# Performance work log

Measured on AMD Instinct MI355X. Metric: run time of the kernel, lower is better.

Reference implementation:

```python
import jax, jax.numpy as jnp
import numpy as np

N_NODES = 100000
N_EDGES = 1600000
N_FEAT = 128
N_HID = 128
N_CLS = 40
DROP_P = 0.5


def setup_inputs() -> dict:
    key = jax.random.key(0)
    k1, k2, k3, k4 = jax.random.split(key, 4)
    x = jax.random.normal(k1, (N_NODES, N_FEAT), dtype=jnp.float32)
    edge_index = jax.random.randint(k2, (2, N_EDGES), 0, N_NODES, dtype=jnp.int32)
    W1 = jax.random.normal(k3, (N_FEAT, N_HID), dtype=jnp.float32) / np.sqrt(N_FEAT)
    b1 = jnp.zeros((N_HID,), dtype=jnp.float32)
    W2 = jax.random.normal(k4, (N_HID, N_CLS), dtype=jnp.float32) / np.sqrt(N_HID)
    b2 = jnp.zeros((N_CLS,), dtype=jnp.float32)
    return {"x": x, "edge_index": edge_index, "W1": W1, "b1": b1, "W2": W2, "b2": b2}


def _gcn_norm(edge_index, num_nodes):
    # add self-loops, then symmetric normalization D^-1/2 (A+I) D^-1/2
    loops = jnp.arange(num_nodes, dtype=edge_index.dtype)
    src = jnp.concatenate([edge_index[0], loops])
    dst = jnp.concatenate([edge_index[1], loops])
    deg = jax.ops.segment_sum(jnp.ones_like(dst, dtype=jnp.float32), dst,
                              num_segments=num_nodes)
    deg_isqrt = jax.lax.rsqrt(deg)  # deg >= 1 thanks to self-loops
    norm = deg_isqrt[src] * deg_isqrt[dst]  # [E+N]
    return src, dst, norm


def _gcn_conv(x, src, dst, norm, W, b, num_nodes):
    h = x @ W                                   # [N, out]
    msg = h[src] * norm[:, None]                # gather + scale, [E+N, out]
    out = jax.ops.segment_sum(msg, dst, num_segments=num_nodes)  # scatter-add
    return out + b


def reference(x, edge_index, W1, b1, W2, b2):
    num_nodes = x.shape[0]
    src, dst, norm = _gcn_norm(edge_index, num_nodes)
    h = _gcn_conv(x, src, dst, norm, W1, b1, num_nodes)
    h = jax.nn.relu(h)
    # dropout(p=0.5, training=True) with a fixed key for determinism
    keep = jax.random.uniform(jax.random.key(42), h.shape) >= DROP_P
    h = jnp.where(keep, h / (1.0 - DROP_P), 0.0)
    out = _gcn_conv(h, src, dst, norm, W2, b2, num_nodes)
    return out
```

## Files before the change

### kernel.cpp

```cpp
#include <hip/hip_runtime.h>

#define N_NODES 100000
#define N_EDGES 1600000
#define NBUCK 196
#define G1B 1563
#define FB 391
#define FEDGE 4096
#define BCAP 9216

typedef __attribute__((ext_vector_type(8))) short short8v;
typedef __attribute__((ext_vector_type(4))) float f32x4;

__device__ __forceinline__ unsigned pack_bf16(float a, float b){
  unsigned ua = __float_as_uint(a), ub = __float_as_uint(b);
  ua = ua + 0x7fffu + ((ua >> 16) & 1u);
  ub = ub + 0x7fffu + ((ub >> 16) & 1u);
  return (ua >> 16) | (ub & 0xffff0000u);
}
__device__ __forceinline__ unsigned short bf16_of(float a){
  unsigned ua = __float_as_uint(a);
  ua = ua + 0x7fffu + ((ua >> 16) & 1u);
  return (unsigned short)(ua >> 16);
}
__device__ __forceinline__ float bf_lo(unsigned u){ return __uint_as_float(u << 16); }
__device__ __forceinline__ float bf_hi(unsigned u){ return __uint_as_float(u & 0xffff0000u); }

__device__ __forceinline__ unsigned tf_rotl(unsigned x, int r){ return (x<<r)|(x>>(32-r)); }

__device__ __forceinline__ unsigned dropout_keep(unsigned e){
  unsigned x0 = 0u, x1 = e;
  const unsigned k0 = 0u, k1v = 42u;
  const unsigned k2 = 0x1BD11BDAu ^ k0 ^ k1v;
#define TF_R(r) { x0 += x1; x1 = tf_rotl(x1,(r)); x1 ^= x0; }
  x0 += k0; x1 += k1v;
  TF_R(13) TF_R(15) TF_R(26) TF_R(6)
  x0 += k1v; x1 += k2 + 1u;
  TF_R(17) TF_R(29) TF_R(16) TF_R(24)
  x0 += k2; x1 += k0 + 2u;
  TF_R(13) TF_R(15) TF_R(26) TF_R(6)
  x0 += k0; x1 += k1v + 3u;
  TF_R(17) TF_R(29) TF_R(16) TF_R(24)
  x0 += k1v; x1 += k2 + 4u;
  TF_R(13) TF_R(15) TF_R(26) TF_R(6)
  x0 += k2; x1 += k0 + 5u;
#undef TF_R
  return (x0 ^ x1) >> 31;
}

__global__ void k_init(const float* __restrict__ W1, const float* __restrict__ W2,
                       unsigned short* __restrict__ W1T, unsigned short* __restrict__ W2T48,
                       int* __restrict__ bcur2){
  int b = blockIdx.x, t = threadIdx.x;
  if (b < 64){
    int idx = b*256 + t;
    int k = idx >> 7, n = idx & 127;
    W1T[n*128 + k] = bf16_of(W1[idx]);
  } else {
    if (t < NBUCK) bcur2[t] = 0;
    for (int i = t; i < 48*128; i += 256){
      int c = i >> 7, k = i & 127;
      W2T48[c*128 + k] = (c < 40) ? bf16_of(W2[k*40 + c]) : (unsigned short)0;
    }
  }
}

__launch_bounds__(256)
__global__ void k_B(const float* __restrict__ x, const unsigned short* __restrict__ W1T,
                    unsigned short* __restrict__ h1u,
                    const int* __restrict__ src, const int* __restrict__ dst,
                    int* __restrict__ bcur2, unsigned* __restrict__ tmp, int N, int E){
  __shared__ int hist[NBUCK];
  int t = threadIdx.x;
  if (blockIdx.x < FB){
    int fb = blockIdx.x;
    for (int i = t; i < NBUCK; i += 256) hist[i] = 0;
    __syncthreads();
    int e0 = fb*FEDGE;
    #pragma unroll 4
    for (int j = 0; j < FEDGE/256; j++){
      int e = e0 + t + j*256;
      if (e < E) atomicAdd(&hist[dst[e] >> 9], 1);
    }
    __syncthreads();
    if (t < NBUCK){
      int c = hist[t];
      if (c > 0) hist[t] = t*BCAP + atomicAdd(&bcur2[t], c);
    }
    __syncthreads();
    #pragma unroll 4
    for (int j = 0; j < FEDGE/256; j++){
      int e = e0 + t + j*256;
      if (e < E){
        int d = dst[e], s = src[e];
        int p = atomicAdd(&hist[d >> 9], 1);
        tmp[p] = ((unsigned)(d & 511) << 17) | (unsigned)s;
      }
    }
    return;
  }
  int gb = blockIdx.x - FB;
  if (gb >= G1B) return;
  int w = t >> 6, l = t & 63;
  int lo = l & 15, hi = l >> 4;
  int rowA = gb*64 + w*16 + lo;
  int rA = (rowA < N) ? rowA : (N-1);
  const float4* xr = (const float4*)(x + (size_t)rA*128);

  short8v a[4];
  #pragma unroll
  for (int kk = 0; kk < 4; kk++){
    float4 f0 = xr[kk*8 + 2*hi];
    float4 f1 = xr[kk*8 + 2*hi + 1];
    union { short8v v; unsigned u[4]; } A;
    A.u[0] = pack_bf16(f0.x, f0.y);
    A.u[1] = pack_bf16(f0.z, f0.w);
    A.u[2] = pack_bf16(f1.x, f1.y);
    A.u[3] = pack_bf16(f1.z, f1.w);
    a[kk] = A.v;
  }
  int rowC0 = gb*64 + w*16 + hi*4;
  #pragma unroll
  for (int tt = 0; tt < 8; tt++){
    int n0 = tt*16;
    const uint4* brow = (const uint4*)(W1T + (n0 + lo)*128);
    f32x4 acc = {0.f, 0.f, 0.f, 0.f};
    #pragma unroll
    for (int kk = 0; kk < 4; kk++){
      union { short8v v; uint4 q; } B;
      B.q = brow[kk*4 + hi];
      acc = __builtin_amdgcn_mfma_f32_16x16x32_bf16(a[kk], B.v, acc, 0, 0, 0);
    }
    int colC = n0 + lo;
    #pragma unroll
    for (int r = 0; r < 4; r++){
      int rc = rowC0 + r;
      if (rc < N) h1u[(size_t)rc*128 + colC] = bf16_of(acc[r]);
    }
  }
}

__launch_bounds__(1024)
__global__ void k_sort(const unsigned* __restrict__ tmp, const int* __restrict__ bcur2,
                       int* __restrict__ degi, int* __restrict__ off,
                       float* __restrict__ dii, unsigned* __restrict__ csr, int N){
  __shared__ int cur[512];
  __shared__ int wtot[8];
  int b = blockIdx.x, t = threadIdx.x;
  if (t < 512) cur[t] = 0;
  __syncthreads();
  int m = bcur2[b];
  int base = b*BCAP;
  int node0 = b << 9;
  for (int i = t; i < m; i += 1024)
    atomicAdd(&cur[tmp[base + i] >> 17], 1);
  __syncthreads();
  int v = 0, excl = 0;
  if (t < 512){
    v = cur[t];
    int lane = t & 63, w = t >> 6;
    int incl = v;
    for (int d = 1; d < 64; d <<= 1){
      int y = __shfl_up(incl, d);
      if (lane >= d) incl += y;
    }
    if (lane == 63) wtot[w] = incl;
    __syncthreads();
    int wb = 0;
    for (int i = 0; i < w; i++) wb += wtot[i];
    excl = wb + incl - v;
    int n = node0 + t;
    if (n < N){
      degi[n] = v;
      off[n]  = base + excl;
      dii[n]  = rsqrtf((float)(v + 1));
    }
  } else {
    __syncthreads();
  }
  __syncthreads();
  if (t < 512) cur[t] = base + excl;
  __syncthreads();
  for (int i = t; i < m; i += 1024){
    unsigned e = tmp[base + i];
    int dloc = e >> 17;
    int p = atomicAdd(&cur[dloc], 1);
    csr[p] = e & 0x1FFFFu;
  }
}

__launch_bounds__(256)
__global__ void k_agg1(const unsigned* __restrict__ h1g, unsigned* __restrict__ Bbg,
                       const unsigned* __restrict__ csr, const int* __restrict__ off,
                       const int* __restrict__ degi, const float* __restrict__ dii,
                       const float* __restrict__ b1, int N){
  int n = blockIdx.x*4 + (threadIdx.x >> 6);
  int lane = threadIdx.x & 63;
  if (n >= N) return;
  n = __builtin_amdgcn_readfirstlane(n);
  float din = dii[n];
  float s2 = din*din;
  unsigned su = h1g[(size_t)n*64 + lane];
  float a0 = bf_lo(su)*s2, a1 = bf_hi(su)*s2;
  int o = off[n], cnt = degi[n];
  int i = 0;
  for (; i + 8 <= cnt; i += 8){
    unsigned s0 = csr[o+i+0], s1 = csr[o+i+1], s2i = csr[o+i+2], s3 = csr[o+i+3];
    unsigned s4 = csr[o+i+4], s5 = csr[o+i+5], s6 = csr[o+i+6], s7 = csr[o+i+7];
    float w0 = dii[s0]*din, w1 = dii[s1]*din, w2 = dii[s2i]*din, w3 = dii[s3]*din;
    float w4 = dii[s4]*din, w5 = dii[s5]*din, w6 = dii[s6]*din, w7 = dii[s7]*din;
    unsigned u0 = h1g[(size_t)s0*64 + lane];
    unsigned u1 = h1g[(size_t)s1*64 + lane];
    unsigned u2 = h1g[(size_t)s2i*64 + lane];
    unsigned u3 = h1g[(size_t)s3*64 + lane];
    unsigned u4 = h1g[(size_t)s4*64 + lane];
    unsigned u5 = h1g[(size_t)s5*64 + lane];
    unsigned u6 = h1g[(size_t)s6*64 + lane];
    unsigned u7 = h1g[(size_t)s7*64 + lane];
    a0 = fmaf(bf_lo(u0), w0, a0); a1 = fmaf(bf_hi(u0), w0, a1);
    a0 = fmaf(bf_lo(u1), w1, a0); a1 = fmaf(bf_hi(u1), w1, a1);
    a0 = fmaf(bf_lo(u2), w2, a0); a1 = fmaf(bf_hi(u2), w2, a1);
    a0 = fmaf(bf_lo(u3), w3, a0); a1 = fmaf(bf_hi(u3), w3, a1);
    a0 = fmaf(bf_lo(u4), w4, a0); a1 = fmaf(bf_hi(u4), w4, a1);
    a0 = fmaf(bf_lo(u5), w5, a0); a1 = fmaf(bf_hi(u5), w5, a1);
    a0 = fmaf(bf_lo(u6), w6, a0); a1 = fmaf(bf_hi(u6), w6, a1);
    a0 = fmaf(bf_lo(u7), w7, a0); a1 = fmaf(bf_hi(u7), w7, a1);
  }
  for (; i < cnt; ++i){
    unsigned s = csr[o+i];
    float w = dii[s]*din;
    unsigned u = h1g[(size_t)s*64 + lane];
    a0 = fmaf(bf_lo(u), w, a0); a1 = fmaf(bf_hi(u), w, a1);
  }
  float2 bb = *(const float2*)(b1 + lane*2);
  a0 = fmaxf(a0 + bb.x, 0.f);
  a1 = fmaxf(a1 + bb.y, 0.f);
  unsigned e0i = (unsigned)n*128u + (unsigned)lane*2u;
  a0 = dropout_keep(e0i)      ? a0*2.f : 0.f;
  a1 = dropout_keep(e0i + 1u) ? a1*2.f : 0.f;
  Bbg[(size_t)n*64 + lane] = pack_bf16(a0, a1);
}

__launch_bounds__(256)
__global__ void k_gemm2(const unsigned* __restrict__ Bbg, const unsigned short* __restrict__ W2T48,
                        unsigned short* __restrict__ h2p, int N){
  int t = threadIdx.x;
  int w = t >> 6, l = t & 63;
  int lo = l & 15, hi = l >> 4;
  int rowA = blockIdx.x*64 + w*16 + lo;
  int rA = (rowA < N) ? rowA : (N-1);
  const uint4* ar = (const uint4*)(Bbg + (size_t)rA*64);

  short8v a[4];
  #pragma unroll
  for (int kk = 0; kk < 4; kk++){
    union { short8v v; uint4 q; } A;
    A.q = ar[kk*4 + hi];
    a[kk] = A.v;
  }
  int rowC0 = blockIdx.x*64 + w*16 + hi*4;
  #pragma unroll
  for (int tt = 0; tt < 3; tt++){
    int n0 = tt*16;
    const uint4* brow = (const uint4*)(W2T48 + (n0 + lo)*128);
    f32x4 acc = {0.f, 0.f, 0.f, 0.f};
    #pragma unroll
    for (int kk = 0; kk < 4; kk++){
      union { short8v v; uint4 q; } B;
      B.q = brow[kk*4 + hi];
      acc = __builtin_amdgcn_mfma_f32_16x16x32_bf16(a[kk], B.v, acc, 0, 0, 0);
    }
    int colC = n0 + lo;
    #pragma unroll
    for (int r = 0; r < 4; r++){
      int rc = rowC0 + r;
      if (rc < N) h2p[(size_t)rc*64 + colC] = bf16_of(acc[r]);
    }
  }
}

__launch_bounds__(256)
__global__ void k_agg2(const unsigned* __restrict__ h2p, float* __restrict__ out,
                       const unsigned* __restrict__ csr, const int* __restrict__ off,
                       const int* __restrict__ degi, const float* __restrict__ dii,
                       const float* __restrict__ b2, int N){
  int n = blockIdx.x*4 + (threadIdx.x >> 6);
  int lane31 = threadIdx.x & 31;
  int lane   = threadIdx.x & 63;
  if (n >= N) return;
  n = __builtin_amdgcn_readfirstlane(n);
  float din = dii[n];
  float sq = din*din;
  unsigned su = h2p[(size_t)n*32 + lane31];
  float a0 = bf_lo(su)*sq, a1 = bf_hi(su)*sq;
  int o = off[n], cnt = degi[n];
  int i = 0;
  for (; i + 8 <= cnt; i += 8){
    unsigned s0 = csr[o+i+0], s1 = csr[o+i+1], s2i = csr[o+i+2], s3 = csr[o+i+3];
    unsigned s4 = csr[o+i+4], s5 = csr[o+i+5], s6 = csr[o+i+6], s7 = csr[o+i+7];
    float w0 = dii[s0]*din, w1 = dii[s1]*din, w2 = dii[s2i]*din, w3 = dii[s3]*din;
    float w4 = dii[s4]*din, w5 = dii[s5]*din, w6 = dii[s6]*din, w7 = dii[s7]*din;
    unsigned u0 = h2p[(size_t)s0*32 + lane31];
    unsigned u1 = h2p[(size_t)s1*32 + lane31];
    unsigned u2 = h2p[(size_t)s2i*32 + lane31];
    unsigned u3 = h2p[(size_t)s3*32 + lane31];
    unsigned u4 = h2p[(size_t)s4*32 + lane31];
    unsigned u5 = h2p[(size_t)s5*32 + lane31];
    unsigned u6 = h2p[(size_t)s6*32 + lane31];
    unsigned u7 = h2p[(size_t)s7*32 + lane31];
    a0 = fmaf(bf_lo(u0), w0, a0); a1 = fmaf(bf_hi(u0), w0, a1);
    a0 = fmaf(bf_lo(u1), w1, a0); a1 = fmaf(bf_hi(u1), w1, a1);
    a0 = fmaf(bf_lo(u2), w2, a0); a1 = fmaf(bf_hi(u2), w2, a1);
    a0 = fmaf(bf_lo(u3), w3, a0); a1 = fmaf(bf_hi(u3), w3, a1);
    a0 = fmaf(bf_lo(u4), w4, a0); a1 = fmaf(bf_hi(u4), w4, a1);
    a0 = fmaf(bf_lo(u5), w5, a0); a1 = fmaf(bf_hi(u5), w5, a1);
    a0 = fmaf(bf_lo(u6), w6, a0); a1 = fmaf(bf_hi(u6), w6, a1);
    a0 = fmaf(bf_lo(u7), w7, a0); a1 = fmaf(bf_hi(u7), w7, a1);
  }
  for (; i < cnt; ++i){
    unsigned s = csr[o+i];
    float w = dii[s]*din;
    unsigned u = h2p[(size_t)s*32 + lane31];
    a0 = fmaf(bf_lo(u), w, a0); a1 = fmaf(bf_hi(u), w, a1);
  }
  if (lane < 20){
    float2 bb = *(const float2*)(b2 + lane*2);
    a0 += bb.x;
    a1 += bb.y;
    *(float2*)(out + (size_t)n*40 + lane*2) = make_float2(a0, a1);
  }
}

extern "C" void kernel_launch(void* const* d_in, const int* in_sizes, int n_in,
                              void* d_out, int out_size, void* d_ws, size_t ws_size,
                              hipStream_t stream){
  const float* x  = (const float*)d_in[0];
  const int*   ei = (const int*)  d_in[1];
  const float* W1 = (const float*)d_in[2];
  const float* b1 = (const float*)d_in[3];
  const float* W2 = (const float*)d_in[4];
  const float* b2 = (const float*)d_in[5];
  float* out = (float*)d_out;
  char* ws = (char*)d_ws;
  const int N = N_NODES, E = N_EDGES;
  const int* srcv = ei;
  const int* dstv = ei + E;

  int*   bcur2 = (int*)  (ws + 0);
  int*   off   = (int*)  (ws + 8192);
  int*   degi  = (int*)  (ws + 417792);
  float* dii   = (float*)(ws + 827392);
  unsigned short* W1T   = (unsigned short*)(ws + 1236992);
  unsigned short* W2T48 = (unsigned short*)(ws + 1269760);
  unsigned* tmp = (unsigned*)(ws + 1290240);
  unsigned* csr = (unsigned*)(ws + 8519680);
  unsigned short* h1u = (unsigned short*)(ws + 16777216);
  unsigned*       h1g = (unsigned*)      (ws + 16777216);
  unsigned short* h2p = (unsigned short*)(ws + 16777216);
  unsigned*       Bbg = (unsigned*)      (ws + 50331648);

  k_init<<<65, 256, 0, stream>>>(W1, W2, W1T, W2T48, bcur2);
  k_B<<<FB + G1B, 256, 0, stream>>>(x, W1T, h1u, srcv, dstv, bcur2, tmp, N, E);
  k_sort<<<NBUCK, 1024, 0, stream>>>(tmp, bcur2, degi, off, dii, csr, N);

  k_agg1 <<<N/4, 256, 0, stream>>>(h1g, Bbg, csr, off, degi, dii, b1, N);
  k_gemm2<<<(N + 63)/64, 256, 0, stream>>>(Bbg, W2T48, h2p, N);
  k_agg2 <<<N/4, 256, 0, stream>>>((const unsigned*)h2p, out, csr, off, degi, dii, b2, N);
}
```

Baseline: 216.0 us.

## Precompute per-edge normalization weights into CSR entries during sort

Splits the bucket sort into a histogram kernel and a scatter kernel. The scatter kernel, having all dii values available, writes (src, weight) pairs where weight = dii[src]*dii[dst]. Both aggregation kernels then read the weight alongside the index and drop the dependent random dii[src] gather. In exchange the CSR doubles in size, there is an extra kernel launch, and the scatter now does the random dii gathers once.

```diff
diff --git a/kernel.cpp b/kernel.cpp
--- a/kernel.cpp
+++ b/kernel.cpp
@@ -140,9 +140,9 @@
 }
 
 __launch_bounds__(1024)
-__global__ void k_sort(const unsigned* __restrict__ tmp, const int* __restrict__ bcur2,
+__global__ void k_hist(const unsigned* __restrict__ tmp, const int* __restrict__ bcur2,
                        int* __restrict__ degi, int* __restrict__ off,
-                       float* __restrict__ dii, unsigned* __restrict__ csr, int N){
+                       float* __restrict__ dii, int N){
   __shared__ int cur[512];
   __shared__ int wtot[8];
   int b = blockIdx.x, t = threadIdx.x;
@@ -154,9 +154,8 @@
   for (int i = t; i < m; i += 1024)
     atomicAdd(&cur[tmp[base + i] >> 17], 1);
   __syncthreads();
-  int v = 0, excl = 0;
   if (t < 512){
-    v = cur[t];
+    int v = cur[t];
     int lane = t & 63, w = t >> 6;
     int incl = v;
     for (int d = 1; d < 64; d <<= 1){
@@ -167,30 +166,45 @@
     __syncthreads();
     int wb = 0;
     for (int i = 0; i < w; i++) wb += wtot[i];
-    excl = wb + incl - v;
+    int excl = wb + incl - v;
     int n = node0 + t;
     if (n < N){
       degi[n] = v;
       off[n]  = base + excl;
       dii[n]  = rsqrtf((float)(v + 1));
     }
-  } else {
-    __syncthreads();
+  }
+}
+
+__launch_bounds__(1024)
+__global__ void k_csort(const unsigned* __restrict__ tmp, int2* __restrict__ csre,
+                        const int* __restrict__ off, const int* __restrict__ bcur2,
+                        const float* __restrict__ dii, int N){
+  __shared__ int   cur[512];
+  __shared__ float dl[512];
+  int b = blockIdx.x, t = threadIdx.x;
+  int node0 = b << 9;
+  if (t < 512){
+    int n = node0 + t;
+    cur[t] = (n < N) ? off[n] : 0;
+    dl[t]  = (n < N) ? dii[n] : 0.f;
   }
   __syncthreads();
-  if (t < 512) cur[t] = base + excl;
-  __syncthreads();
+  int m = bcur2[b];
+  int base = b*BCAP;
   for (int i = t; i < m; i += 1024){
     unsigned e = tmp[base + i];
     int dloc = e >> 17;
+    int s = e & 0x1FFFFu;
+    float w = dii[s] * dl[dloc];
     int p = atomicAdd(&cur[dloc], 1);
-    csr[p] = e & 0x1FFFFu;
+    csre[p] = make_int2(s, __float_as_int(w));
   }
 }
 
 __launch_bounds__(256)
 __global__ void k_agg1(const unsigned* __restrict__ h1g, unsigned* __restrict__ Bbg,
-                       const unsigned* __restrict__ csr, const int* __restrict__ off,
+                       const int2* __restrict__ csre, const int* __restrict__ off,
                        const int* __restrict__ degi, const float* __restrict__ dii,
                        const float* __restrict__ b1, int N){
   int n = blockIdx.x*4 + (threadIdx.x >> 6);
@@ -204,18 +218,20 @@
   int o = off[n], cnt = degi[n];
   int i = 0;
   for (; i + 8 <= cnt; i += 8){
-    unsigned s0 = csr[o+i+0], s1 = csr[o+i+1], s2i = csr[o+i+2], s3 = csr[o+i+3];
-    unsigned s4 = csr[o+i+4], s5 = csr[o+i+5], s6 = csr[o+i+6], s7 = csr[o+i+7];
-    float w0 = dii[s0]*din, w1 = dii[s1]*din, w2 = dii[s2i]*din, w3 = dii[s3]*din;
-    float w4 = dii[s4]*din, w5 = dii[s5]*din, w6 = dii[s6]*din, w7 = dii[s7]*din;
-    unsigned u0 = h1g[(size_t)s0*64 + lane];
-    unsigned u1 = h1g[(size_t)s1*64 + lane];
-    unsigned u2 = h1g[(size_t)s2i*64 + lane];
-    unsigned u3 = h1g[(size_t)s3*64 + lane];
-    unsigned u4 = h1g[(size_t)s4*64 + lane];
-    unsigned u5 = h1g[(size_t)s5*64 + lane];
-    unsigned u6 = h1g[(size_t)s6*64 + lane];
-    unsigned u7 = h1g[(size_t)s7*64 + lane];
+    int2 e0 = csre[o+i+0], e1 = csre[o+i+1], e2 = csre[o+i+2], e3 = csre[o+i+3];
+    int2 e4 = csre[o+i+4], e5 = csre[o+i+5], e6 = csre[o+i+6], e7 = csre[o+i+7];
+    unsigned u0 = h1g[(size_t)e0.x*64 + lane];
+    unsigned u1 = h1g[(size_t)e1.x*64 + lane];
+    unsigned u2 = h1g[(size_t)e2.x*64 + lane];
+    unsigned u3 = h1g[(size_t)e3.x*64 + lane];
+    unsigned u4 = h1g[(size_t)e4.x*64 + lane];
+    unsigned u5 = h1g[(size_t)e5.x*64 + lane];
+    unsigned u6 = h1g[(size_t)e6.x*64 + lane];
+    unsigned u7 = h1g[(size_t)e7.x*64 + lane];
+    float w0 = __int_as_float(e0.y), w1 = __int_as_float(e1.y);
+    float w2 = __int_as_float(e2.y), w3 = __int_as_float(e3.y);
+    float w4 = __int_as_float(e4.y), w5 = __int_as_float(e5.y);
+    float w6 = __int_as_float(e6.y), w7 = __int_as_float(e7.y);
     a0 = fmaf(bf_lo(u0), w0, a0); a1 = fmaf(bf_hi(u0), w0, a1);
     a0 = fmaf(bf_lo(u1), w1, a0); a1 = fmaf(bf_hi(u1), w1, a1);
     a0 = fmaf(bf_lo(u2), w2, a0); a1 = fmaf(bf_hi(u2), w2, a1);
@@ -226,9 +242,9 @@
     a0 = fmaf(bf_lo(u7), w7, a0); a1 = fmaf(bf_hi(u7), w7, a1);
   }
   for (; i < cnt; ++i){
-    unsigned s = csr[o+i];
-    float w = dii[s]*din;
-    unsigned u = h1g[(size_t)s*64 + lane];
+    int2 e = csre[o+i];
+    unsigned u = h1g[(size_t)e.x*64 + lane];
+    float w = __int_as_float(e.y);
     a0 = fmaf(bf_lo(u), w, a0); a1 = fmaf(bf_hi(u), w, a1);
   }
   float2 bb = *(const float2*)(b1 + lane*2);
@@ -280,7 +296,7 @@
 
 __launch_bounds__(256)
 __global__ void k_agg2(const unsigned* __restrict__ h2p, float* __restrict__ out,
-                       const unsigned* __restrict__ csr, const int* __restrict__ off,
+                       const int2* __restrict__ csre, const int* __restrict__ off,
                        const int* __restrict__ degi, const float* __restrict__ dii,
                        const float* __restrict__ b2, int N){
   int n = blockIdx.x*4 + (threadIdx.x >> 6);
@@ -295,18 +311,20 @@
   int o = off[n], cnt = degi[n];
   int i = 0;
   for (; i + 8 <= cnt; i += 8){
-    unsigned s0 = csr[o+i+0], s1 = csr[o+i+1], s2i = csr[o+i+2], s3 = csr[o+i+3];
-    unsigned s4 = csr[o+i+4], s5 = csr[o+i+5], s6 = csr[o+i+6], s7 = csr[o+i+7];
-    float w0 = dii[s0]*din, w1 = dii[s1]*din, w2 = dii[s2i]*din, w3 = dii[s3]*din;
-    float w4 = dii[s4]*din, w5 = dii[s5]*din, w6 = dii[s6]*din, w7 = dii[s7]*din;
-    unsigned u0 = h2p[(size_t)s0*32 + lane31];
-    unsigned u1 = h2p[(size_t)s1*32 + lane31];
-    unsigned u2 = h2p[(size_t)s2i*32 + lane31];
-    unsigned u3 = h2p[(size_t)s3*32 + lane31];
-    unsigned u4 = h2p[(size_t)s4*32 + lane31];
-    unsigned u5 = h2p[(size_t)s5*32 + lane31];
-    unsigned u6 = h2p[(size_t)s6*32 + lane31];
-    unsigned u7 = h2p[(size_t)s7*32 + lane31];
+    int2 e0 = csre[o+i+0], e1 = csre[o+i+1], e2 = csre[o+i+2], e3 = csre[o+i+3];
+    int2 e4 = csre[o+i+4], e5 = csre[o+i+5], e6 = csre[o+i+6], e7 = csre[o+i+7];
+    unsigned u0 = h2p[(size_t)e0.x*32 + lane31];
+    unsigned u1 = h2p[(size_t)e1.x*32 + lane31];
+    unsigned u2 = h2p[(size_t)e2.x*32 + lane31];
+    unsigned u3 = h2p[(size_t)e3.x*32 + lane31];
+    unsigned u4 = h2p[(size_t)e4.x*32 + lane31];
+    unsigned u5 = h2p[(size_t)e5.x*32 + lane31];
+    unsigned u6 = h2p[(size_t)e6.x*32 + lane31];
+    unsigned u7 = h2p[(size_t)e7.x*32 + lane31];
+    float w0 = __int_as_float(e0.y), w1 = __int_as_float(e1.y);
+    float w2 = __int_as_float(e2.y), w3 = __int_as_float(e3.y);
+    float w4 = __int_as_float(e4.y), w5 = __int_as_float(e5.y);
+    float w6 = __int_as_float(e6.y), w7 = __int_as_float(e7.y);
     a0 = fmaf(bf_lo(u0), w0, a0); a1 = fmaf(bf_hi(u0), w0, a1);
     a0 = fmaf(bf_lo(u1), w1, a0); a1 = fmaf(bf_hi(u1), w1, a1);
     a0 = fmaf(bf_lo(u2), w2, a0); a1 = fmaf(bf_hi(u2), w2, a1);
@@ -317,9 +335,9 @@
     a0 = fmaf(bf_lo(u7), w7, a0); a1 = fmaf(bf_hi(u7), w7, a1);
   }
   for (; i < cnt; ++i){
-    unsigned s = csr[o+i];
-    float w = dii[s]*din;
-    unsigned u = h2p[(size_t)s*32 + lane31];
+    int2 e = csre[o+i];
+    unsigned u = h2p[(size_t)e.x*32 + lane31];
+    float w = __int_as_float(e.y);
     a0 = fmaf(bf_lo(u), w, a0); a1 = fmaf(bf_hi(u), w, a1);
   }
   if (lane < 20){
@@ -352,17 +370,18 @@
   unsigned short* W1T   = (unsigned short*)(ws + 1236992);
   unsigned short* W2T48 = (unsigned short*)(ws + 1269760);
   unsigned* tmp = (unsigned*)(ws + 1290240);
-  unsigned* csr = (unsigned*)(ws + 8519680);
-  unsigned short* h1u = (unsigned short*)(ws + 16777216);
-  unsigned*       h1g = (unsigned*)      (ws + 16777216);
-  unsigned short* h2p = (unsigned short*)(ws + 16777216);
-  unsigned*       Bbg = (unsigned*)      (ws + 50331648);
+  int2*     csre= (int2*)   (ws + 8519680);
+  unsigned short* h1u = (unsigned short*)(ws + 23068672);
+  unsigned*       h1g = (unsigned*)      (ws + 23068672);
+  unsigned short* h2p = (unsigned short*)(ws + 23068672);
+  unsigned*       Bbg = (unsigned*)      (ws + 56623104);
 
   k_init<<<65, 256, 0, stream>>>(W1, W2, W1T, W2T48, bcur2);
   k_B<<<FB + G1B, 256, 0, stream>>>(x, W1T, h1u, srcv, dstv, bcur2, tmp, N, E);
-  k_sort<<<NBUCK, 1024, 0, stream>>>(tmp, bcur2, degi, off, dii, csr, N);
-
-  k_agg1 <<<N/4, 256, 0, stream>>>(h1g, Bbg, csr, off, degi, dii, b1, N);
+  k_hist<<<NBUCK, 1024, 0, stream>>>(tmp, bcur2, degi, off, dii, N);
+  k_csort<<<NBUCK, 1024, 0, stream>>>(tmp, csre, off, bcur2, dii, N);
+
+  k_agg1 <<<N/4, 256, 0, stream>>>(h1g, Bbg, csre, off, degi, dii, b1, N);
   k_gemm2<<<(N + 63)/64, 256, 0, stream>>>(Bbg, W2T48, h2p, N);
-  k_agg2 <<<N/4, 256, 0, stream>>>((const unsigned*)h2p, out, csr, off, degi, dii, b2, N);
-}
+  k_agg2 <<<N/4, 256, 0, stream>>>((const unsigned*)h2p, out, csre, off, degi, dii, b2, N);
+}
```

New measurement: 210.5 us. 1.03x faster.
